# Kernel optimization log

Hardware: AMD Instinct MI355X
Metric: run time of the kernel (lower is better)

The kernel has to match this reference:

```python
import jax, jax.numpy as jnp
import numpy as np

EMBED_DIM = 512
NUM_JOINTS = 17
HIDDEN = EMBED_DIM * 2  # hidden_ratio=2
B, T = 32, 243


def setup_inputs() -> dict:
    key = jax.random.key(0)
    k_x, k_w1, k_w2 = jax.random.split(key, 3)
    x = jax.random.normal(k_x, (B, T, NUM_JOINTS, EMBED_DIM), dtype=jnp.float32)
    # kaiming_uniform with a=sqrt(5): bound = sqrt(6 / ((1 + a^2) * fan_in)) = sqrt(1/fan_in)
    b1 = float(np.sqrt(1.0 / EMBED_DIM))
    fc1_w = jax.random.uniform(k_w1, (NUM_JOINTS, EMBED_DIM, HIDDEN), minval=-b1, maxval=b1, dtype=jnp.float32)
    fc1_b = jnp.zeros((NUM_JOINTS, HIDDEN), dtype=jnp.float32)
    b2 = float(np.sqrt(1.0 / HIDDEN))
    fc2_w = jax.random.uniform(k_w2, (NUM_JOINTS, HIDDEN, 3), minval=-b2, maxval=b2, dtype=jnp.float32)
    fc2_b = jnp.zeros((NUM_JOINTS, 3), dtype=jnp.float32)
    ln_gamma = jnp.ones((EMBED_DIM,), dtype=jnp.float32)
    ln_beta = jnp.zeros((EMBED_DIM,), dtype=jnp.float32)
    return {"x": x, "ln_gamma": ln_gamma, "ln_beta": ln_beta,
            "fc1_w": fc1_w, "fc1_b": fc1_b, "fc2_w": fc2_w, "fc2_b": fc2_b}


def _layernorm(x, gamma, beta, eps=1e-5):
    mu = jnp.mean(x, axis=-1, keepdims=True)
    var = jnp.mean(jnp.square(x - mu), axis=-1, keepdims=True)
    return (x - mu) * jax.lax.rsqrt(var + eps) * gamma + beta


def reference(x, ln_gamma, ln_beta, fc1_w, fc1_b, fc2_w, fc2_b):
    # x: [B, T, J, d] -> [B, T, J, 3]
    xn = _layernorm(x, ln_gamma, ln_beta)
    h = jnp.einsum('btjd,jdh->btjh', xn, fc1_w) + fc1_b  # [B,T,J,H]
    h = jax.nn.gelu(h, approximate=False)  # torch GELU default is exact (erf)
    y = jnp.einsum('btjh,jho->btjo', h, fc2_w) + fc2_b  # [B,T,J,3]
    return y
```

## Files before the change

### kernel.cpp

```cpp
#include <hip/hip_runtime.h>
#include <hip/hip_bf16.h>

#define JN   17
#define DIM  512
#define HID  1024
#define MTOT 7776
#define BN   256
#define BK   32
#define NTHR 512

typedef __attribute__((ext_vector_type(8))) short s16x8;
typedef __attribute__((ext_vector_type(4))) float f32x4;
typedef unsigned short ushort_t;

__device__ __forceinline__ unsigned int f2bf(float f) {
    return (unsigned int)__builtin_bit_cast(unsigned short, __float2bfloat16(f));
}

__device__ __forceinline__ float gelu_erf(float h) {
    float ah = fabsf(h);
    float z  = ah * 0.7071067811865476f;
    float t  = __builtin_amdgcn_rcpf(fmaf(0.3275911f, z, 1.0f));
    float p  = fmaf(fmaf(fmaf(fmaf(1.061405429f, t, -1.453152027f), t,
                              1.421413741f), t, -0.284496736f), t, 0.254829592f);
    float er = 1.0f - p * t * __expf(-z * z);
    return fmaf(0.5f * ah, er, 0.5f * h);
}

__global__ __launch_bounds__(256)
void prep_w1(const float* __restrict__ w1, ushort_t* __restrict__ w1s) {
    int b  = blockIdx.x;
    int nq = b & 3;
    int kc = (b >> 2) & 15;
    int j  = b >> 6;
    int n  = nq * 256 + threadIdx.x;

    const float* src = w1 + ((size_t)j * DIM + kc * 32) * HID + n;
    ushort_t* dst = w1s + (((size_t)j * 16 + kc) * 1024 + n) * 32;

    #pragma unroll
    for (int u = 0; u < 4; ++u) {
        float v[8];
        #pragma unroll
        for (int e = 0; e < 8; ++e) v[e] = src[(u * 8 + e) * HID];
        uint4 qq;
        qq.x = f2bf(v[0]) | (f2bf(v[1]) << 16);
        qq.y = f2bf(v[2]) | (f2bf(v[3]) << 16);
        qq.z = f2bf(v[4]) | (f2bf(v[5]) << 16);
        qq.w = f2bf(v[6]) | (f2bf(v[7]) << 16);
        int p = u ^ ((n >> 1) & 3);
        *(uint4*)(dst + p * 8) = qq;
    }
}

#define BM3 96
#define A3_OFF 0
#define B3_OFF 98304
#define Y3_OFF 98304
#define SMEM_V3 163840

__global__ __launch_bounds__(NTHR, 2)
void pjh_fused_v3(const float* __restrict__ x,
                  const float* __restrict__ gamma,
                  const float* __restrict__ beta,
                  const ushort_t* __restrict__ w1s,
                  const float* __restrict__ b1,
                  const float* __restrict__ w2,
                  const float* __restrict__ b2,
                  float* __restrict__ out)
{
    extern __shared__ char smem[];
    const int tid  = threadIdx.x;
    const int lane = tid & 63;
    const int wv   = tid >> 6;
    const int wm   = wv >> 2;
    const int wn   = wv & 3;
    const int mt   = blockIdx.x;
    const int j    = blockIdx.y;

    const ushort_t* w1j = w1s + (size_t)j * 16 * 1024 * 32;

    #pragma unroll
    for (int tt = 0; tt < 2; ++tt) {
        int kc = tt & 15, nt = 0;
        const ushort_t* tb = w1j + ((size_t)kc * 1024 + nt * 256) * 32;
        #pragma unroll
        for (int q = 0; q < 2; ++q) {
            const ushort_t* src = tb + (size_t)(wv * 2 + q) * 512 + lane * 8;
            void* dst = smem + B3_OFF + tt * 16384 + (wv * 2 + q) * 1024;
            __builtin_amdgcn_global_load_lds(
                (const __attribute__((address_space(1))) unsigned int*)src,
                (__attribute__((address_space(3))) unsigned int*)dst, 16, 0, 0);
        }
    }

    {
        const float4* gp  = (const float4*)(gamma + lane * 8);
        const float4* bpp = (const float4*)(beta + lane * 8);
        float4 g0 = gp[0], g1 = gp[1];
        float4 e0 = bpp[0], e1 = bpp[1];
        #pragma unroll
        for (int rb = 0; rb < 12; rb += 4) {
            float4 xs[4][2];
            #pragma unroll
            for (int r = 0; r < 4; ++r) {
                int gr = mt * BM3 + wv * 12 + rb + r;
                const float4* xp = (const float4*)(x + ((size_t)gr * JN + j) * DIM + lane * 8);
                xs[r][0] = xp[0]; xs[r][1] = xp[1];
            }
            #pragma unroll
            for (int r = 0; r < 4; ++r) {
                int m = wv * 12 + rb + r;
                float4 xa = xs[r][0], xb = xs[r][1];
                float s  = ((xa.x + xa.y) + (xa.z + xa.w)) + ((xb.x + xb.y) + (xb.z + xb.w));
                float s2 = fmaf(xa.x, xa.x, fmaf(xa.y, xa.y, fmaf(xa.z, xa.z, fmaf(xa.w, xa.w,
                           fmaf(xb.x, xb.x, fmaf(xb.y, xb.y, fmaf(xb.z, xb.z, xb.w * xb.w)))))));
                #pragma unroll
                for (int d = 1; d < 64; d <<= 1) {
                    s  += __shfl_xor(s,  d);
                    s2 += __shfl_xor(s2, d);
                }
                float mu  = s * (1.0f / 512.0f);
                float var = s2 * (1.0f / 512.0f) - mu * mu;
                float rs  = rsqrtf(var + 1e-5f);
                float v0 = fmaf((xa.x - mu) * rs, g0.x, e0.x);
                float v1 = fmaf((xa.y - mu) * rs, g0.y, e0.y);
                float v2 = fmaf((xa.z - mu) * rs, g0.z, e0.z);
                float v3 = fmaf((xa.w - mu) * rs, g0.w, e0.w);
                float v4 = fmaf((xb.x - mu) * rs, g1.x, e1.x);
                float v5 = fmaf((xb.y - mu) * rs, g1.y, e1.y);
                float v6 = fmaf((xb.z - mu) * rs, g1.z, e1.z);
                float v7 = fmaf((xb.w - mu) * rs, g1.w, e1.w);
                uint4 qq;
                qq.x = f2bf(v0) | (f2bf(v1) << 16);
                qq.y = f2bf(v2) | (f2bf(v3) << 16);
                qq.z = f2bf(v4) | (f2bf(v5) << 16);
                qq.w = f2bf(v6) | (f2bf(v7) << 16);
                *(uint4*)(smem + A3_OFF + m * 1024 + ((lane ^ (m & 7)) * 16)) = qq;
            }
        }
    }

    __syncthreads();

    float yr[3][4][3];
    #pragma unroll
    for (int a = 0; a < 3; ++a)
        #pragma unroll
        for (int r = 0; r < 4; ++r)
            #pragma unroll
            for (int o = 0; o < 3; ++o) yr[a][r][o] = 0.f;

    const f32x4 zero4 = {0.f, 0.f, 0.f, 0.f};
    f32x4 acc[3][4];
    #pragma unroll
    for (int mf = 0; mf < 3; ++mf)
        #pragma unroll
        for (int nf = 0; nf < 4; ++nf) acc[mf][nf] = zero4;

    #pragma unroll 1
    for (int t = 0; t < 64; ++t) {
        if (t + 2 < 64) {
            int kc = (t + 2) & 15, nt = (t + 2) >> 4;
            const ushort_t* tb = w1j + ((size_t)kc * 1024 + nt * 256) * 32;
            int bb = ((t + 2) & 3) * 16384;
            #pragma unroll
            for (int q = 0; q < 2; ++q) {
                const ushort_t* src = tb + (size_t)(wv * 2 + q) * 512 + lane * 8;
                void* dst = smem + B3_OFF + bb + (wv * 2 + q) * 1024;
                __builtin_amdgcn_global_load_lds(
                    (const __attribute__((address_space(1))) unsigned int*)src,
                    (__attribute__((address_space(3))) unsigned int*)dst, 16, 0, 0);
            }
        }

        int kc = t & 15;
        int bb = (t & 3) * 16384;
        int g  = lane >> 4;
        s16x8 aF[3], bF[4];
        #pragma unroll
        for (int mf = 0; mf < 3; ++mf) {
            int m  = wm * 48 + mf * 16 + (lane & 15);
            int ul = kc * 4 + g;
            aF[mf] = *(const s16x8*)(smem + A3_OFF + m * 1024 + ((ul ^ (m & 7)) * 16));
        }
        #pragma unroll
        for (int nf = 0; nf < 4; ++nf) {
            int nl = wn * 64 + nf * 16 + (lane & 15);
            int p  = g ^ ((nl >> 1) & 3);
            bF[nf] = *(const s16x8*)(smem + B3_OFF + bb + (nl * 4 + p) * 16);
        }

        __builtin_amdgcn_s_setprio(1);
        #pragma unroll
        for (int mf = 0; mf < 3; ++mf)
            #pragma unroll
            for (int nf = 0; nf < 4; ++nf)
                acc[mf][nf] = __builtin_amdgcn_mfma_f32_16x16x32_bf16(aF[mf], bF[nf], acc[mf][nf], 0, 0, 0);
        __builtin_amdgcn_s_setprio(0);

        if ((t & 15) == 15) {
            int nt = t >> 4;
            #pragma unroll
            for (int nf = 0; nf < 4; ++nf) {
                int n = nt * BN + wn * 64 + nf * 16 + (lane & 15);
                float b1v = b1[j * HID + n];
                const float* w2p = w2 + ((size_t)j * HID + n) * 3;
                float w20 = w2p[0], w21 = w2p[1], w22 = w2p[2];
                #pragma unroll
                for (int mf = 0; mf < 3; ++mf) {
                    #pragma unroll
                    for (int r = 0; r < 4; ++r) {
                        float gv = gelu_erf(acc[mf][nf][r] + b1v);
                        yr[mf][r][0] = fmaf(gv, w20, yr[mf][r][0]);
                        yr[mf][r][1] = fmaf(gv, w21, yr[mf][r][1]);
                        yr[mf][r][2] = fmaf(gv, w22, yr[mf][r][2]);
                    }
                }
            }
            #pragma unroll
            for (int mf = 0; mf < 3; ++mf)
                #pragma unroll
                for (int nf = 0; nf < 4; ++nf)
                    acc[mf][nf] = zero4;
        }

        if (t < 62) {
            asm volatile("s_waitcnt vmcnt(2)" ::: "memory");
        } else {
            asm volatile("s_waitcnt vmcnt(0)" ::: "memory");
        }
        __builtin_amdgcn_s_barrier();
    }

    #pragma unroll
    for (int mf = 0; mf < 3; ++mf)
        #pragma unroll
        for (int r = 0; r < 4; ++r)
            #pragma unroll
            for (int o = 0; o < 3; ++o) {
                float v = yr[mf][r][o];
                v += __shfl_xor(v, 1);
                v += __shfl_xor(v, 2);
                v += __shfl_xor(v, 4);
                v += __shfl_xor(v, 8);
                yr[mf][r][o] = v;
            }

    __syncthreads();

    float* Yp = (float*)(smem + Y3_OFF);
    if ((lane & 15) == 0) {
        int mrow = lane >> 4;
        #pragma unroll
        for (int mf = 0; mf < 3; ++mf)
            #pragma unroll
            for (int r = 0; r < 4; ++r) {
                int m = wm * 48 + mf * 16 + mrow * 4 + r;
                #pragma unroll
                for (int o = 0; o < 3; ++o)
                    Yp[(wn * BM3 + m) * 3 + o] = yr[mf][r][o];
            }
    }
    __syncthreads();

    if (tid < BM3 * 3) {
        int m = tid / 3;
        int o = tid - m * 3;
        int gr = mt * BM3 + m;
        float v = Yp[m * 3 + o] + Yp[(BM3 + m) * 3 + o]
                + Yp[(2 * BM3 + m) * 3 + o] + Yp[(3 * BM3 + m) * 3 + o]
                + b2[j * 3 + o];
        out[((size_t)gr * JN + j) * 3 + o] = v;
    }
}

#define BM   128
#define A1_OFF 0
#define B1_OFF 131072
#define Y1_OFF 147456
#define SMEM_V1 153600

__global__ __launch_bounds__(NTHR, 2)
void pjh_fused_v1(const float* __restrict__ x,
                  const float* __restrict__ gamma,
                  const float* __restrict__ beta,
                  const float* __restrict__ w1,
                  const float* __restrict__ b1,
                  const float* __restrict__ w2,
                  const float* __restrict__ b2,
                  float* __restrict__ out)
{
    extern __shared__ char smem[];
    const int tid  = threadIdx.x;
    const int lane = tid & 63;
    const int wv   = tid >> 6;
    const int wm   = wv >> 2;
    const int wn   = wv & 3;
    const int mt   = blockIdx.x;
    const int j    = blockIdx.y;
    const int t2 = tid >> 7;
    const int n2 = (tid & 127) * 2;
    const float* w1j = w1 + (size_t)j * DIM * HID;

    float la[8][2];
    {
        const float* bp = w1j + (size_t)(8 * t2) * HID + n2;
        #pragma unroll
        for (int i = 0; i < 8; ++i) { la[i][0] = bp[i * HID + 0]; la[i][1] = bp[i * HID + 1]; }
    }
    {
        const float4* gp = (const float4*)(gamma + lane * 8);
        const float4* bpp = (const float4*)(beta + lane * 8);
        float4 g0 = gp[0], g1 = gp[1];
        float4 e0 = bpp[0], e1 = bpp[1];
        #pragma unroll 1
        for (int rr = 0; rr < 16; ++rr) {
            int m  = wv * 16 + rr;
            int gr = mt * BM + m;
            float4 xa = {0.f,0.f,0.f,0.f}, xb = {0.f,0.f,0.f,0.f};
            if (gr < MTOT) {
                const float4* xp = (const float4*)(x + ((size_t)gr * JN + j) * DIM + lane * 8);
                xa = xp[0]; xb = xp[1];
            }
            float s  = ((xa.x + xa.y) + (xa.z + xa.w)) + ((xb.x + xb.y) + (xb.z + xb.w));
            float s2 = fmaf(xa.x, xa.x, fmaf(xa.y, xa.y, fmaf(xa.z, xa.z, fmaf(xa.w, xa.w,
                       fmaf(xb.x, xb.x, fmaf(xb.y, xb.y, fmaf(xb.z, xb.z, xb.w * xb.w)))))));
            #pragma unroll
            for (int d = 1; d < 64; d <<= 1) { s += __shfl_xor(s, d); s2 += __shfl_xor(s2, d); }
            float mu  = s * (1.0f / 512.0f);
            float var = s2 * (1.0f / 512.0f) - mu * mu;
            float rs  = rsqrtf(var + 1e-5f);
            uint4 qq = {0u,0u,0u,0u};
            if (gr < MTOT) {
                float v0 = fmaf((xa.x - mu) * rs, g0.x, e0.x);
                float v1 = fmaf((xa.y - mu) * rs, g0.y, e0.y);
                float v2 = fmaf((xa.z - mu) * rs, g0.z, e0.z);
                float v3 = fmaf((xa.w - mu) * rs, g0.w, e0.w);
                float v4 = fmaf((xb.x - mu) * rs, g1.x, e1.x);
                float v5 = fmaf((xb.y - mu) * rs, g1.y, e1.y);
                float v6 = fmaf((xb.z - mu) * rs, g1.z, e1.z);
                float v7 = fmaf((xb.w - mu) * rs, g1.w, e1.w);
                qq.x = f2bf(v0) | (f2bf(v1) << 16);
                qq.y = f2bf(v2) | (f2bf(v3) << 16);
                qq.z = f2bf(v4) | (f2bf(v5) << 16);
                qq.w = f2bf(v6) | (f2bf(v7) << 16);
            }
            *(uint4*)(smem + A1_OFF + m * 1024 + ((lane ^ (m & 7)) * 16)) = qq;
        }
    }

    float yr[4][4][3];
    #pragma unroll
    for (int a = 0; a < 4; ++a)
        #pragma unroll
        for (int r = 0; r < 4; ++r)
            #pragma unroll
            for (int o = 0; o < 3; ++o) yr[a][r][o] = 0.f;
    const f32x4 zero4 = {0.f,0.f,0.f,0.f};

    #pragma unroll 1
    for (int nt = 0; nt < 4; ++nt) {
        f32x4 acc[4][4];
        #pragma unroll
        for (int mf = 0; mf < 4; ++mf)
            #pragma unroll
            for (int nf = 0; nf < 4; ++nf) acc[mf][nf] = zero4;
        #pragma unroll 1
        for (int kci = 0; kci < 16; ++kci) {
            __syncthreads();
            #pragma unroll
            for (int u = 0; u < 2; ++u) {
                int n = n2 + u;
                uint4 qq;
                qq.x = f2bf(la[0][u]) | (f2bf(la[1][u]) << 16);
                qq.y = f2bf(la[2][u]) | (f2bf(la[3][u]) << 16);
                qq.z = f2bf(la[4][u]) | (f2bf(la[5][u]) << 16);
                qq.w = f2bf(la[6][u]) | (f2bf(la[7][u]) << 16);
                int phys = t2 ^ ((n >> 1) & 3);
                *(uint4*)(smem + B1_OFF + n * 64 + phys * 16) = qq;
            }
            __syncthreads();
            int gt = nt * 16 + kci;
            if (gt + 1 < 64) {
                int nnt = (gt + 1) >> 4;
                int nkc = ((gt + 1) & 15) * BK;
                const float* bp = w1j + (size_t)(nkc + 8 * t2) * HID + nnt * BN + n2;
                #pragma unroll
                for (int i = 0; i < 8; ++i) { la[i][0] = bp[i * HID + 0]; la[i][1] = bp[i * HID + 1]; }
            }
            int kc = kci * BK;
            s16x8 aF[4], bF[4];
            #pragma unroll
            for (int mf = 0; mf < 4; ++mf) {
                int m  = wm * 64 + mf * 16 + (lane & 15);
                int ul = (kc >> 3) + (lane >> 4);
                aF[mf] = *(const s16x8*)(smem + A1_OFF + m * 1024 + ((ul ^ (m & 7)) * 16));
            }
            #pragma unroll
            for (int nf = 0; nf < 4; ++nf) {
                int n  = wn * 64 + nf * 16 + (lane & 15);
                int ph = (lane >> 4) ^ ((n >> 1) & 3);
                bF[nf] = *(const s16x8*)(smem + B1_OFF + n * 64 + ph * 16);
            }
            #pragma unroll
            for (int mf = 0; mf < 4; ++mf)
                #pragma unroll
                for (int nf = 0; nf < 4; ++nf)
                    acc[mf][nf] = __builtin_amdgcn_mfma_f32_16x16x32_bf16(aF[mf], bF[nf], acc[mf][nf], 0, 0, 0);
        }
        #pragma unroll
        for (int nf = 0; nf < 4; ++nf) {
            int n = nt * BN + wn * 64 + nf * 16 + (lane & 15);
            float b1v = b1[j * HID + n];
            const float* w2p = w2 + ((size_t)j * HID + n) * 3;
            float w20 = w2p[0], w21 = w2p[1], w22 = w2p[2];
            #pragma unroll
            for (int mf = 0; mf < 4; ++mf)
                #pragma unroll
                for (int r = 0; r < 4; ++r) {
                    float gv = gelu_erf(acc[mf][nf][r] + b1v);
                    yr[mf][r][0] = fmaf(gv, w20, yr[mf][r][0]);
                    yr[mf][r][1] = fmaf(gv, w21, yr[mf][r][1]);
                    yr[mf][r][2] = fmaf(gv, w22, yr[mf][r][2]);
                }
        }
    }
    #pragma unroll
    for (int mf = 0; mf < 4; ++mf)
        #pragma unroll
        for (int r = 0; r < 4; ++r)
            #pragma unroll
            for (int o = 0; o < 3; ++o) {
                float v = yr[mf][r][o];
                v += __shfl_xor(v, 1); v += __shfl_xor(v, 2);
                v += __shfl_xor(v, 4); v += __shfl_xor(v, 8);
                yr[mf][r][o] = v;
            }
    float* Yp = (float*)(smem + Y1_OFF);
    if ((lane & 15) == 0) {
        int mrow = lane >> 4;
        #pragma unroll
        for (int mf = 0; mf < 4; ++mf)
            #pragma unroll
            for (int r = 0; r < 4; ++r) {
                int m = wm * 64 + mf * 16 + mrow * 4 + r;
                #pragma unroll
                for (int o = 0; o < 3; ++o) Yp[(wn * BM + m) * 3 + o] = yr[mf][r][o];
            }
    }
    __syncthreads();
    if (tid < BM * 3) {
        int m = tid / 3;
        int o = tid - m * 3;
        int gr = mt * BM + m;
        if (gr < MTOT) {
            float v = Yp[m * 3 + o] + Yp[(BM + m) * 3 + o]
                    + Yp[(2 * BM + m) * 3 + o] + Yp[(3 * BM + m) * 3 + o]
                    + b2[j * 3 + o];
            out[((size_t)gr * JN + j) * 3 + o] = v;
        }
    }
}

extern "C" void kernel_launch(void* const* d_in, const int* in_sizes, int n_in,
                              void* d_out, int out_size, void* d_ws, size_t ws_size,
                              hipStream_t stream) {
    (void)in_sizes; (void)n_in; (void)out_size;
    const float* x   = (const float*)d_in[0];
    const float* ga  = (const float*)d_in[1];
    const float* be  = (const float*)d_in[2];
    const float* w1  = (const float*)d_in[3];
    const float* b1  = (const float*)d_in[4];
    const float* w2  = (const float*)d_in[5];
    const float* b2  = (const float*)d_in[6];
    float* out = (float*)d_out;

    const size_t w1s_bytes = (size_t)JN * 16 * 1024 * 4 * 8 * sizeof(ushort_t);

    if (ws_size >= w1s_bytes) {
        ushort_t* w1s = (ushort_t*)d_ws;
        prep_w1<<<JN * 16 * 4, 256, 0, stream>>>(w1, w1s);
        hipFuncSetAttribute((const void*)pjh_fused_v3,
                            hipFuncAttributeMaxDynamicSharedMemorySize, SMEM_V3);
        dim3 grid(MTOT / BM3, JN);
        pjh_fused_v3<<<grid, NTHR, SMEM_V3, stream>>>(x, ga, be, w1s, b1, w2, b2, out);
    } else {
        hipFuncSetAttribute((const void*)pjh_fused_v1,
                            hipFuncAttributeMaxDynamicSharedMemorySize, SMEM_V1);
        dim3 grid((MTOT + BM - 1) / BM, JN);
        pjh_fused_v1<<<grid, NTHR, SMEM_V1, stream>>>(x, ga, be, w1, b1, w2, b2, out);
    }
}
```

Baseline: 328.6 us.

## Split LayerNorm into prep kernel and stream A tiles through triple-buffered GEMM

```diff
diff --git a/kernel.cpp b/kernel.cpp
--- a/kernel.cpp
+++ b/kernel.cpp
@@ -5,8 +5,8 @@
 #define DIM  512
 #define HID  1024
 #define MTOT 7776
+#define MPAD 7808
 #define BN   256
-#define BK   32
 #define NTHR 512
 
 typedef __attribute__((ext_vector_type(8))) short s16x8;
@@ -51,6 +51,230 @@
         int p = u ^ ((n >> 1) & 3);
         *(uint4*)(dst + p * 8) = qq;
     }
+}
+
+__global__ __launch_bounds__(NTHR)
+void prep_xn(const float* __restrict__ x,
+             const float* __restrict__ gamma,
+             const float* __restrict__ beta,
+             ushort_t* __restrict__ xa)
+{
+    const int lane = threadIdx.x & 63;
+    const int wv   = threadIdx.x >> 6;
+    const int m    = blockIdx.x * 8 + wv;
+    const int j    = blockIdx.y;
+
+    const float4* gp = (const float4*)(gamma + lane * 8);
+    const float4* bp = (const float4*)(beta + lane * 8);
+    float4 g0 = gp[0], g1 = gp[1];
+    float4 e0 = bp[0], e1 = bp[1];
+
+    const float4* xp = (const float4*)(x + ((size_t)m * JN + j) * DIM + lane * 8);
+    float4 va = xp[0], vb = xp[1];
+
+    float s  = ((va.x + va.y) + (va.z + va.w)) + ((vb.x + vb.y) + (vb.z + vb.w));
+    float s2 = fmaf(va.x, va.x, fmaf(va.y, va.y, fmaf(va.z, va.z, fmaf(va.w, va.w,
+               fmaf(vb.x, vb.x, fmaf(vb.y, vb.y, fmaf(vb.z, vb.z, vb.w * vb.w)))))));
+    #pragma unroll
+    for (int d = 1; d < 64; d <<= 1) {
+        s  += __shfl_xor(s,  d);
+        s2 += __shfl_xor(s2, d);
+    }
+    float mu  = s * (1.0f / 512.0f);
+    float var = s2 * (1.0f / 512.0f) - mu * mu;
+    float rs  = rsqrtf(var + 1e-5f);
+
+    float v0 = fmaf((va.x - mu) * rs, g0.x, e0.x);
+    float v1 = fmaf((va.y - mu) * rs, g0.y, e0.y);
+    float v2 = fmaf((va.z - mu) * rs, g0.z, e0.z);
+    float v3 = fmaf((va.w - mu) * rs, g0.w, e0.w);
+    float v4 = fmaf((vb.x - mu) * rs, g1.x, e1.x);
+    float v5 = fmaf((vb.y - mu) * rs, g1.y, e1.y);
+    float v6 = fmaf((vb.z - mu) * rs, g1.z, e1.z);
+    float v7 = fmaf((vb.w - mu) * rs, g1.w, e1.w);
+    uint4 qq;
+    qq.x = f2bf(v0) | (f2bf(v1) << 16);
+    qq.y = f2bf(v2) | (f2bf(v3) << 16);
+    qq.z = f2bf(v4) | (f2bf(v5) << 16);
+    qq.w = f2bf(v6) | (f2bf(v7) << 16);
+
+    int kc = lane >> 2;
+    int p  = (lane & 3) ^ (m & 3) ^ ((m >> 2) & 3);
+    *(uint4*)(xa + (((size_t)j * 16 + kc) * MPAD + m) * 32 + p * 8) = qq;
+}
+
+#define SLOT   24576
+#define BOFF   8192
+#define SMEM_V4 73728
+
+__global__ __launch_bounds__(NTHR, 4)
+void pjh_gemm_v4(const ushort_t* __restrict__ xa,
+                 const ushort_t* __restrict__ w1s,
+                 const float* __restrict__ b1,
+                 const float* __restrict__ w2,
+                 const float* __restrict__ b2,
+                 float* __restrict__ out)
+{
+    extern __shared__ char smem[];
+    const int tid  = threadIdx.x;
+    const int lane = tid & 63;
+    const int wv   = tid >> 6;
+    const int wm   = wv >> 2;
+    const int wn   = wv & 3;
+    const int mt   = blockIdx.x;
+    const int j    = blockIdx.y;
+
+    const ushort_t* xaj = xa  + (size_t)j * 16 * MPAD * 32;
+    const ushort_t* w1j = w1s + (size_t)j * 16 * 1024 * 32;
+
+#define ISSUE(TT, SS) {                                                        \
+        int kc_ = (TT) & 15, nt_ = (TT) >> 4;                                  \
+        const ushort_t* as_ = xaj + ((size_t)kc_ * MPAD + mt * 128) * 32 + tid * 8; \
+        __builtin_amdgcn_global_load_lds(                                      \
+            (const __attribute__((address_space(1))) unsigned int*)as_,        \
+            (__attribute__((address_space(3))) unsigned int*)(smem + (SS) * SLOT + wv * 1024), \
+            16, 0, 0);                                                         \
+        const ushort_t* bs_ = w1j + ((size_t)kc_ * 1024 + nt_ * 256) * 32;     \
+        _Pragma("unroll")                                                      \
+        for (int q_ = 0; q_ < 2; ++q_) {                                       \
+            const ushort_t* src_ = bs_ + (size_t)(wv * 2 + q_) * 512 + lane * 8; \
+            __builtin_amdgcn_global_load_lds(                                  \
+                (const __attribute__((address_space(1))) unsigned int*)src_,   \
+                (__attribute__((address_space(3))) unsigned int*)(smem + (SS) * SLOT + BOFF + (wv * 2 + q_) * 1024), \
+                16, 0, 0);                                                     \
+        }                                                                      \
+    }
+
+    float yr[4][4][3];
+    #pragma unroll
+    for (int a = 0; a < 4; ++a)
+        #pragma unroll
+        for (int r = 0; r < 4; ++r)
+            #pragma unroll
+            for (int o = 0; o < 3; ++o) yr[a][r][o] = 0.f;
+
+    const f32x4 zero4 = {0.f, 0.f, 0.f, 0.f};
+    f32x4 acc[4][4];
+    #pragma unroll
+    for (int mf = 0; mf < 4; ++mf)
+        #pragma unroll
+        for (int nf = 0; nf < 4; ++nf) acc[mf][nf] = zero4;
+
+    ISSUE(0, 0);
+    ISSUE(1, 1);
+    asm volatile("s_waitcnt vmcnt(3)" ::: "memory");
+    __builtin_amdgcn_s_barrier();
+
+    int sr = 0;
+    #pragma unroll 1
+    for (int t = 0; t < 64; ++t) {
+        int sw = sr + 2; if (sw >= 3) sw -= 3;
+        if (t + 2 < 64) ISSUE(t + 2, sw);
+
+        const char* Abase = smem + sr * SLOT;
+        const char* Bbase = smem + sr * SLOT + BOFF;
+        const int g = lane >> 4;
+
+        s16x8 aF[4], bF[4];
+        #pragma unroll
+        for (int mf = 0; mf < 4; ++mf) {
+            int ml = wm * 64 + mf * 16 + (lane & 15);
+            int p  = g ^ (ml & 3) ^ ((ml >> 2) & 3);
+            aF[mf] = *(const s16x8*)(Abase + ml * 64 + p * 16);
+        }
+        #pragma unroll
+        for (int nf = 0; nf < 4; ++nf) {
+            int nl = wn * 64 + nf * 16 + (lane & 15);
+            int p  = g ^ ((nl >> 1) & 3);
+            bF[nf] = *(const s16x8*)(Bbase + (nl * 4 + p) * 16);
+        }
+
+        __builtin_amdgcn_s_setprio(1);
+        #pragma unroll
+        for (int mf = 0; mf < 4; ++mf)
+            #pragma unroll
+            for (int nf = 0; nf < 4; ++nf)
+                acc[mf][nf] = __builtin_amdgcn_mfma_f32_16x16x32_bf16(aF[mf], bF[nf], acc[mf][nf], 0, 0, 0);
+        __builtin_amdgcn_s_setprio(0);
+
+        if ((t & 15) == 15) {
+            int nt = t >> 4;
+            #pragma unroll
+            for (int nf = 0; nf < 4; ++nf) {
+                int n = nt * BN + wn * 64 + nf * 16 + (lane & 15);
+                float b1v = b1[j * HID + n];
+                const float* w2p = w2 + ((size_t)j * HID + n) * 3;
+                float w20 = w2p[0], w21 = w2p[1], w22 = w2p[2];
+                #pragma unroll
+                for (int mf = 0; mf < 4; ++mf) {
+                    #pragma unroll
+                    for (int r = 0; r < 4; ++r) {
+                        float gv = gelu_erf(acc[mf][nf][r] + b1v);
+                        yr[mf][r][0] = fmaf(gv, w20, yr[mf][r][0]);
+                        yr[mf][r][1] = fmaf(gv, w21, yr[mf][r][1]);
+                        yr[mf][r][2] = fmaf(gv, w22, yr[mf][r][2]);
+                    }
+                }
+            }
+            #pragma unroll
+            for (int mf = 0; mf < 4; ++mf)
+                #pragma unroll
+                for (int nf = 0; nf < 4; ++nf)
+                    acc[mf][nf] = zero4;
+        }
+
+        if (t < 62) {
+            asm volatile("s_waitcnt vmcnt(3)" ::: "memory");
+        } else {
+            asm volatile("s_waitcnt vmcnt(0)" ::: "memory");
+        }
+        __builtin_amdgcn_s_barrier();
+        ++sr; if (sr >= 3) sr -= 3;
+    }
+
+    #pragma unroll
+    for (int mf = 0; mf < 4; ++mf)
+        #pragma unroll
+        for (int r = 0; r < 4; ++r)
+            #pragma unroll
+            for (int o = 0; o < 3; ++o) {
+                float v = yr[mf][r][o];
+                v += __shfl_xor(v, 1);
+                v += __shfl_xor(v, 2);
+                v += __shfl_xor(v, 4);
+                v += __shfl_xor(v, 8);
+                yr[mf][r][o] = v;
+            }
+
+    __syncthreads();
+
+    float* Yp = (float*)smem;
+    if ((lane & 15) == 0) {
+        int mrow = lane >> 4;
+        #pragma unroll
+        for (int mf = 0; mf < 4; ++mf)
+            #pragma unroll
+            for (int r = 0; r < 4; ++r) {
+                int m = wm * 64 + mf * 16 + mrow * 4 + r;
+                #pragma unroll
+                for (int o = 0; o < 3; ++o)
+                    Yp[(wn * 128 + m) * 3 + o] = yr[mf][r][o];
+            }
+    }
+    __syncthreads();
+
+    if (tid < 128 * 3) {
+        int m = tid / 3;
+        int o = tid - m * 3;
+        int gr = mt * 128 + m;
+        if (gr < MTOT) {
+            float v = Yp[m * 3 + o] + Yp[(128 + m) * 3 + o]
+                    + Yp[(2 * 128 + m) * 3 + o] + Yp[(3 * 128 + m) * 3 + o]
+                    + b2[j * 3 + o];
+            out[((size_t)gr * JN + j) * 3 + o] = v;
+        }
+    }
+#undef ISSUE
 }
 
 #define BM3 96
@@ -82,8 +306,7 @@
 
     #pragma unroll
     for (int tt = 0; tt < 2; ++tt) {
-        int kc = tt & 15, nt = 0;
-        const ushort_t* tb = w1j + ((size_t)kc * 1024 + nt * 256) * 32;
+        const ushort_t* tb = w1j + (size_t)tt * 1024 * 32;
         #pragma unroll
         for (int q = 0; q < 2; ++q) {
             const ushort_t* src = tb + (size_t)(wv * 2 + q) * 512 + lane * 8;
@@ -111,10 +334,10 @@
             #pragma unroll
             for (int r = 0; r < 4; ++r) {
                 int m = wv * 12 + rb + r;
-                float4 xa = xs[r][0], xb = xs[r][1];
-                float s  = ((xa.x + xa.y) + (xa.z + xa.w)) + ((xb.x + xb.y) + (xb.z + xb.w));
-                float s2 = fmaf(xa.x, xa.x, fmaf(xa.y, xa.y, fmaf(xa.z, xa.z, fmaf(xa.w, xa.w,
-                           fmaf(xb.x, xb.x, fmaf(xb.y, xb.y, fmaf(xb.z, xb.z, xb.w * xb.w)))))));
+                float4 va = xs[r][0], vb = xs[r][1];
+                float s  = ((va.x + va.y) + (va.z + va.w)) + ((vb.x + vb.y) + (vb.z + vb.w));
+                float s2 = fmaf(va.x, va.x, fmaf(va.y, va.y, fmaf(va.z, va.z, fmaf(va.w, va.w,
+                           fmaf(vb.x, vb.x, fmaf(vb.y, vb.y, fmaf(vb.z, vb.z, vb.w * vb.w)))))));
                 #pragma unroll
                 for (int d = 1; d < 64; d <<= 1) {
                     s  += __shfl_xor(s,  d);
@@ -123,14 +346,14 @@
                 float mu  = s * (1.0f / 512.0f);
                 float var = s2 * (1.0f / 512.0f) - mu * mu;
                 float rs  = rsqrtf(var + 1e-5f);
-                float v0 = fmaf((xa.x - mu) * rs, g0.x, e0.x);
-                float v1 = fmaf((xa.y - mu) * rs, g0.y, e0.y);
-                float v2 = fmaf((xa.z - mu) * rs, g0.z, e0.z);
-                float v3 = fmaf((xa.w - mu) * rs, g0.w, e0.w);
-                float v4 = fmaf((xb.x - mu) * rs, g1.x, e1.x);
-                float v5 = fmaf((xb.y - mu) * rs, g1.y, e1.y);
-                float v6 = fmaf((xb.z - mu) * rs, g1.z, e1.z);
-                float v7 = fmaf((xb.w - mu) * rs, g1.w, e1.w);
+                float v0 = fmaf((va.x - mu) * rs, g0.x, e0.x);
+                float v1 = fmaf((va.y - mu) * rs, g0.y, e0.y);
+                float v2 = fmaf((va.z - mu) * rs, g0.z, e0.z);
+                float v3 = fmaf((va.w - mu) * rs, g0.w, e0.w);
+                float v4 = fmaf((vb.x - mu) * rs, g1.x, e1.x);
+                float v5 = fmaf((vb.y - mu) * rs, g1.y, e1.y);
+                float v6 = fmaf((vb.z - mu) * rs, g1.z, e1.z);
+                float v7 = fmaf((vb.w - mu) * rs, g1.w, e1.w);
                 uint4 qq;
                 qq.x = f2bf(v0) | (f2bf(v1) << 16);
                 qq.y = f2bf(v2) | (f2bf(v3) << 16);
@@ -272,194 +495,6 @@
                 + Yp[(2 * BM3 + m) * 3 + o] + Yp[(3 * BM3 + m) * 3 + o]
                 + b2[j * 3 + o];
         out[((size_t)gr * JN + j) * 3 + o] = v;
-    }
-}
-
-#define BM   128
-#define A1_OFF 0
-#define B1_OFF 131072
-#define Y1_OFF 147456
-#define SMEM_V1 153600
-
-__global__ __launch_bounds__(NTHR, 2)
-void pjh_fused_v1(const float* __restrict__ x,
-                  const float* __restrict__ gamma,
-                  const float* __restrict__ beta,
-                  const float* __restrict__ w1,
-                  const float* __restrict__ b1,
-                  const float* __restrict__ w2,
-                  const float* __restrict__ b2,
-                  float* __restrict__ out)
-{
-    extern __shared__ char smem[];
-    const int tid  = threadIdx.x;
-    const int lane = tid & 63;
-    const int wv   = tid >> 6;
-    const int wm   = wv >> 2;
-    const int wn   = wv & 3;
-    const int mt   = blockIdx.x;
-    const int j    = blockIdx.y;
-    const int t2 = tid >> 7;
-    const int n2 = (tid & 127) * 2;
-    const float* w1j = w1 + (size_t)j * DIM * HID;
-
-    float la[8][2];
-    {
-        const float* bp = w1j + (size_t)(8 * t2) * HID + n2;
-        #pragma unroll
-        for (int i = 0; i < 8; ++i) { la[i][0] = bp[i * HID + 0]; la[i][1] = bp[i * HID + 1]; }
-    }
-    {
-        const float4* gp = (const float4*)(gamma + lane * 8);
-        const float4* bpp = (const float4*)(beta + lane * 8);
-        float4 g0 = gp[0], g1 = gp[1];
-        float4 e0 = bpp[0], e1 = bpp[1];
-        #pragma unroll 1
-        for (int rr = 0; rr < 16; ++rr) {
-            int m  = wv * 16 + rr;
-            int gr = mt * BM + m;
-            float4 xa = {0.f,0.f,0.f,0.f}, xb = {0.f,0.f,0.f,0.f};
-            if (gr < MTOT) {
-                const float4* xp = (const float4*)(x + ((size_t)gr * JN + j) * DIM + lane * 8);
-                xa = xp[0]; xb = xp[1];
-            }
-            float s  = ((xa.x + xa.y) + (xa.z + xa.w)) + ((xb.x + xb.y) + (xb.z + xb.w));
-            float s2 = fmaf(xa.x, xa.x, fmaf(xa.y, xa.y, fmaf(xa.z, xa.z, fmaf(xa.w, xa.w,
-                       fmaf(xb.x, xb.x, fmaf(xb.y, xb.y, fmaf(xb.z, xb.z, xb.w * xb.w)))))));
-            #pragma unroll
-            for (int d = 1; d < 64; d <<= 1) { s += __shfl_xor(s, d); s2 += __shfl_xor(s2, d); }
-            float mu  = s * (1.0f / 512.0f);
-            float var = s2 * (1.0f / 512.0f) - mu * mu;
-            float rs  = rsqrtf(var + 1e-5f);
-            uint4 qq = {0u,0u,0u,0u};
-            if (gr < MTOT) {
-                float v0 = fmaf((xa.x - mu) * rs, g0.x, e0.x);
-                float v1 = fmaf((xa.y - mu) * rs, g0.y, e0.y);
-                float v2 = fmaf((xa.z - mu) * rs, g0.z, e0.z);
-                float v3 = fmaf((xa.w - mu) * rs, g0.w, e0.w);
-                float v4 = fmaf((xb.x - mu) * rs, g1.x, e1.x);
-                float v5 = fmaf((xb.y - mu) * rs, g1.y, e1.y);
-                float v6 = fmaf((xb.z - mu) * rs, g1.z, e1.z);
-                float v7 = fmaf((xb.w - mu) * rs, g1.w, e1.w);
-                qq.x = f2bf(v0) | (f2bf(v1) << 16);
-                qq.y = f2bf(v2) | (f2bf(v3) << 16);
-                qq.z = f2bf(v4) | (f2bf(v5) << 16);
-                qq.w = f2bf(v6) | (f2bf(v7) << 16);
-            }
-            *(uint4*)(smem + A1_OFF + m * 1024 + ((lane ^ (m & 7)) * 16)) = qq;
-        }
-    }
-
-    float yr[4][4][3];
-    #pragma unroll
-    for (int a = 0; a < 4; ++a)
-        #pragma unroll
-        for (int r = 0; r < 4; ++r)
-            #pragma unroll
-            for (int o = 0; o < 3; ++o) yr[a][r][o] = 0.f;
-    const f32x4 zero4 = {0.f,0.f,0.f,0.f};
-
-    #pragma unroll 1
-    for (int nt = 0; nt < 4; ++nt) {
-        f32x4 acc[4][4];
-        #pragma unroll
-        for (int mf = 0; mf < 4; ++mf)
-            #pragma unroll
-            for (int nf = 0; nf < 4; ++nf) acc[mf][nf] = zero4;
-        #pragma unroll 1
-        for (int kci = 0; kci < 16; ++kci) {
-            __syncthreads();
-            #pragma unroll
-            for (int u = 0; u < 2; ++u) {
-                int n = n2 + u;
-                uint4 qq;
-                qq.x = f2bf(la[0][u]) | (f2bf(la[1][u]) << 16);
-                qq.y = f2bf(la[2][u]) | (f2bf(la[3][u]) << 16);
-                qq.z = f2bf(la[4][u]) | (f2bf(la[5][u]) << 16);
-                qq.w = f2bf(la[6][u]) | (f2bf(la[7][u]) << 16);
-                int phys = t2 ^ ((n >> 1) & 3);
-                *(uint4*)(smem + B1_OFF + n * 64 + phys * 16) = qq;
-            }
-            __syncthreads();
-            int gt = nt * 16 + kci;
-            if (gt + 1 < 64) {
-                int nnt = (gt + 1) >> 4;
-                int nkc = ((gt + 1) & 15) * BK;
-                const float* bp = w1j + (size_t)(nkc + 8 * t2) * HID + nnt * BN + n2;
-                #pragma unroll
-                for (int i = 0; i < 8; ++i) { la[i][0] = bp[i * HID + 0]; la[i][1] = bp[i * HID + 1]; }
-            }
-            int kc = kci * BK;
-            s16x8 aF[4], bF[4];
-            #pragma unroll
-            for (int mf = 0; mf < 4; ++mf) {
-                int m  = wm * 64 + mf * 16 + (lane & 15);
-                int ul = (kc >> 3) + (lane >> 4);
-                aF[mf] = *(const s16x8*)(smem + A1_OFF + m * 1024 + ((ul ^ (m & 7)) * 16));
-            }
-            #pragma unroll
-            for (int nf = 0; nf < 4; ++nf) {
-                int n  = wn * 64 + nf * 16 + (lane & 15);
-                int ph = (lane >> 4) ^ ((n >> 1) & 3);
-                bF[nf] = *(const s16x8*)(smem + B1_OFF + n * 64 + ph * 16);
-            }
-            #pragma unroll
-            for (int mf = 0; mf < 4; ++mf)
-                #pragma unroll
-                for (int nf = 0; nf < 4; ++nf)
-                    acc[mf][nf] = __builtin_amdgcn_mfma_f32_16x16x32_bf16(aF[mf], bF[nf], acc[mf][nf], 0, 0, 0);
-        }
-        #pragma unroll
-        for (int nf = 0; nf < 4; ++nf) {
-            int n = nt * BN + wn * 64 + nf * 16 + (lane & 15);
-            float b1v = b1[j * HID + n];
-            const float* w2p = w2 + ((size_t)j * HID + n) * 3;
-            float w20 = w2p[0], w21 = w2p[1], w22 = w2p[2];
-            #pragma unroll
-            for (int mf = 0; mf < 4; ++mf)
-                #pragma unroll
-                for (int r = 0; r < 4; ++r) {
-                    float gv = gelu_erf(acc[mf][nf][r] + b1v);
-                    yr[mf][r][0] = fmaf(gv, w20, yr[mf][r][0]);
-                    yr[mf][r][1] = fmaf(gv, w21, yr[mf][r][1]);
-                    yr[mf][r][2] = fmaf(gv, w22, yr[mf][r][2]);
-                }
-        }
-    }
-    #pragma unroll
-    for (int mf = 0; mf < 4; ++mf)
-        #pragma unroll
-        for (int r = 0; r < 4; ++r)
-            #pragma unroll
-            for (int o = 0; o < 3; ++o) {
-                float v = yr[mf][r][o];
-                v += __shfl_xor(v, 1); v += __shfl_xor(v, 2);
-                v += __shfl_xor(v, 4); v += __shfl_xor(v, 8);
-                yr[mf][r][o] = v;
-            }
-    float* Yp = (float*)(smem + Y1_OFF);
-    if ((lane & 15) == 0) {
-        int mrow = lane >> 4;
-        #pragma unroll
-        for (int mf = 0; mf < 4; ++mf)
-            #pragma unroll
-            for (int r = 0; r < 4; ++r) {
-                int m = wm * 64 + mf * 16 + mrow * 4 + r;
-                #pragma unroll
-                for (int o = 0; o < 3; ++o) Yp[(wn * BM + m) * 3 + o] = yr[mf][r][o];
-            }
-    }
-    __syncthreads();
-    if (tid < BM * 3) {
-        int m = tid / 3;
-        int o = tid - m * 3;
-        int gr = mt * BM + m;
-        if (gr < MTOT) {
-            float v = Yp[m * 3 + o] + Yp[(BM + m) * 3 + o]
-                    + Yp[(2 * BM + m) * 3 + o] + Yp[(3 * BM + m) * 3 + o]
-                    + b2[j * 3 + o];
-            out[((size_t)gr * JN + j) * 3 + o] = v;
-        }
     }
 }
 
@@ -476,19 +511,24 @@
     const float* b2  = (const float*)d_in[6];
     float* out = (float*)d_out;
 
-    const size_t w1s_bytes = (size_t)JN * 16 * 1024 * 4 * 8 * sizeof(ushort_t);
-
-    if (ws_size >= w1s_bytes) {
+    const size_t xa_bytes  = (size_t)JN * 16 * MPAD * 32 * sizeof(ushort_t);
+    const size_t w1s_bytes = (size_t)JN * 16 * 1024 * 32 * sizeof(ushort_t);
+
+    if (ws_size >= xa_bytes + w1s_bytes) {
+        ushort_t* xa  = (ushort_t*)d_ws;
+        ushort_t* w1s = (ushort_t*)((char*)d_ws + xa_bytes);
+        prep_xn<<<dim3(MTOT / 8, JN), NTHR, 0, stream>>>(x, ga, be, xa);
+        prep_w1<<<JN * 16 * 4, 256, 0, stream>>>(w1, w1s);
+        hipFuncSetAttribute((const void*)pjh_gemm_v4,
+                            hipFuncAttributeMaxDynamicSharedMemorySize, SMEM_V4);
+        dim3 grid(MPAD / 128, JN);
+        pjh_gemm_v4<<<grid, NTHR, SMEM_V4, stream>>>(xa, w1s, b1, w2, b2, out);
+    } else {
         ushort_t* w1s = (ushort_t*)d_ws;
         prep_w1<<<JN * 16 * 4, 256, 0, stream>>>(w1, w1s);
         hipFuncSetAttribute((const void*)pjh_fused_v3,
                             hipFuncAttributeMaxDynamicSharedMemorySize, SMEM_V3);
         dim3 grid(MTOT / BM3, JN);
         pjh_fused_v3<<<grid, NTHR, SMEM_V3, stream>>>(x, ga, be, w1s, b1, w2, b2, out);
-    } else {
-        hipFuncSetAttribute((const void*)pjh_fused_v1,
-                            hipFuncAttributeMaxDynamicSharedMemorySize, SMEM_V1);
-        dim3 grid((MTOT + BM - 1) / BM, JN);
-        pjh_fused_v1<<<grid, NTHR, SMEM_V1, stream>>>(x, ga, be, w1, b1, w2, b2, out);
-    }
-}
+    }
+}
```

After: 605.9 us. 84.4% more time.
